# Optimization experiments

Hardware: AMD Instinct MI355X
Metric: run time of the kernel (lower is better)

The kernel has to match this reference:

```python
import jax, jax.numpy as jnp
import numpy as np

HIDDEN = 3584
H = 28          # num attention heads
KV = 4          # num key-value heads
HD = 128        # head dim
MROPE = [16, 24, 24]  # sum*2 == HD
EPS = 1e-6
S_TOT = 4096
N_SAMPLES = 4


def rmsnorm(x, w, eps=EPS):
    return x * jax.lax.rsqrt(jnp.mean(x * x, axis=-1, keepdims=True) + eps) * w


def rotate_half(x):
    x1, x2 = jnp.split(x, 2, axis=-1)
    return jnp.concatenate([-x2, x1], axis=-1)


def mrope_merge(t):
    # t: [3, S, HD] -> [S, HD], section i taken from rope axis i%3
    cuts = np.cumsum(np.array(MROPE) * 2)[:-1]
    parts = jnp.split(t, cuts, axis=-1)
    return jnp.concatenate([p[i % 3] for i, p in enumerate(parts)], axis=-1)


def setup_inputs() -> dict:
    key = jax.random.key(0)
    ks = iter(jax.random.split(key, 32))
    std = 0.02

    def w(shape):
        return jax.random.normal(next(ks), shape, dtype=jnp.float32) * std

    inp = {
        "packed_sequence": jax.random.normal(next(ks), (S_TOT, HIDDEN), dtype=jnp.float32),
        "packed_cos": jax.random.uniform(next(ks), (3, S_TOT, HD), dtype=jnp.float32, minval=-1.0, maxval=1.0),
        "packed_sin": jax.random.uniform(next(ks), (3, S_TOT, HD), dtype=jnp.float32, minval=-1.0, maxval=1.0),
    }
    # und / geo indices partition [0, S_TOT)
    inp["packed_und_token_indexes"] = jnp.arange(S_TOT // 2, dtype=jnp.int64 if jax.config.jax_enable_x64 else jnp.int32)
    inp["packed_geo_token_indexes"] = jnp.arange(S_TOT // 2, dtype=inp["packed_und_token_indexes"].dtype) + S_TOT // 2
    inp["sample_len"] = S_TOT // N_SAMPLES

    for tag in ("und", "geo"):
        inp[f"q_w_{tag}"] = w((H * HD, HIDDEN))
        inp[f"q_b_{tag}"] = jnp.zeros((H * HD,), jnp.float32)
        inp[f"k_w_{tag}"] = w((KV * HD, HIDDEN))
        inp[f"k_b_{tag}"] = jnp.zeros((KV * HD,), jnp.float32)
        inp[f"v_w_{tag}"] = w((KV * HD, HIDDEN))
        inp[f"v_b_{tag}"] = jnp.zeros((KV * HD,), jnp.float32)
        inp[f"o_w_{tag}"] = w((HIDDEN, H * HD))
        inp[f"q_norm_{tag}"] = jnp.ones((HD,), jnp.float32)
        inp[f"k_norm_{tag}"] = jnp.ones((HD,), jnp.float32)
    return inp


def reference(packed_sequence, packed_cos, packed_sin,
              q_w_und, q_b_und, k_w_und, k_b_und, v_w_und, v_b_und, o_w_und,
              q_norm_und, k_norm_und,
              q_w_geo, q_b_geo, k_w_geo, k_b_geo, v_w_geo, v_b_geo, o_w_geo,
              q_norm_geo, k_norm_geo,
              packed_und_token_indexes, packed_geo_token_indexes, sample_len):
    S, D = packed_sequence.shape
    G = H // KV
    und, geo = packed_und_token_indexes, packed_geo_token_indexes
    xu = packed_sequence[und]
    xg = packed_sequence[geo]

    def scatter(dim, fu, fg):
        out = jnp.zeros((S, dim), packed_sequence.dtype)
        return out.at[und].set(fu).at[geo].set(fg)

    # modality-routed QKV projections (gather -> gemm -> scatter)
    q = scatter(H * HD, xu @ q_w_und.T + q_b_und, xg @ q_w_geo.T + q_b_geo).reshape(S, H, HD)
    k = scatter(KV * HD, xu @ k_w_und.T + k_b_und, xg @ k_w_geo.T + k_b_geo).reshape(S, KV, HD)
    v = scatter(KV * HD, xu @ v_w_und.T + v_b_und, xg @ v_w_geo.T + v_b_geo).reshape(S, KV, HD)

    # per-modality QK RMSNorm
    qn = jnp.zeros_like(q).at[und].set(rmsnorm(q[und], q_norm_und)).at[geo].set(rmsnorm(q[geo], q_norm_geo))
    kn = jnp.zeros_like(k).at[und].set(rmsnorm(k[und], k_norm_und)).at[geo].set(rmsnorm(k[geo], k_norm_geo))

    # multimodal rotary embedding
    cos = mrope_merge(packed_cos)[:, None, :]  # [S,1,HD]
    sin = mrope_merge(packed_sin)[:, None, :]
    qr = qn * cos + rotate_half(qn) * sin
    kr = kn * cos + rotate_half(kn) * sin

    # block-diagonal causal attention over packed equal-length samples
    L = int(sample_len)
    B = S // L
    qb = qr.reshape(B, L, H, HD)
    kb = jnp.repeat(kr.reshape(B, L, KV, HD), G, axis=2)  # GQA expansion
    vb = jnp.repeat(v.reshape(B, L, KV, HD), G, axis=2)
    scores = jnp.einsum('blhd,bmhd->bhlm', qb, kb) / np.sqrt(HD).astype(np.float32)
    causal = jnp.tril(jnp.ones((L, L), bool))
    scores = jnp.where(causal, scores, jnp.finfo(scores.dtype).min)
    attn = jax.nn.softmax(scores, axis=-1)
    out = jnp.einsum('bhlm,bmhd->blhd', attn, vb).reshape(S, H * HD)

    # modality-routed output projection
    res = jnp.zeros((S, D), packed_sequence.dtype)
    res = res.at[und].set(out[und] @ o_w_und.T).at[geo].set(out[geo] @ o_w_geo.T)
    return res
```

## Files before the change

kernel.cpp:

```cpp
#include <hip/hip_runtime.h>
#include <hip/hip_bf16.h>
#include <stdint.h>

#define HIDDEN 3584
#define NH 28
#define NKV 4
#define HD 128
#define GQ (NH / NKV)
#define NQKV ((NH + 2 * NKV) * HD)
#define LSAMP 1024

typedef __bf16 bf16x8 __attribute__((ext_vector_type(8)));
typedef float f32x4 __attribute__((ext_vector_type(4)));

__device__ __forceinline__ unsigned short f2bf(float f) {
  unsigned int u = __float_as_uint(f);
  u += 0x7fffu + ((u >> 16) & 1u);
  return (unsigned short)(u >> 16);
}
__device__ __forceinline__ float bf2f(unsigned short h) {
  return __uint_as_float(((unsigned int)h) << 16);
}

__device__ __forceinline__ void gload16(const void* g, void* l) {
  __builtin_amdgcn_global_load_lds(
      (const __attribute__((address_space(1))) void*)g,
      (__attribute__((address_space(3))) void*)l, 16, 0, 0);
}

__global__ void build_maps_kernel(const int* __restrict__ und, const int* __restrict__ geo,
                                  int nu, int ng,
                                  int* __restrict__ row_of_token, int* __restrict__ tok_of_row,
                                  int* __restrict__ mod_of_token) {
  int i = blockIdx.x * 256 + threadIdx.x;
  if (i < nu) {
    int t = und[i];
    row_of_token[t] = i; tok_of_row[i] = t; mod_of_token[t] = 0;
  } else if (i < nu + ng) {
    int j = i - nu;
    int t = geo[j];
    row_of_token[t] = nu + j; tok_of_row[nu + j] = t; mod_of_token[t] = 1;
  }
}

struct Cvt8 {
  const float* src[8];
  unsigned short* dst[8];
  int cum[8];
};
__global__ void convert8_kernel(Cvt8 a, int tot4) {
  int i = blockIdx.x * blockDim.x + threadIdx.x;
  const int stride = gridDim.x * blockDim.x;
  for (; i < tot4; i += stride) {
    int seg = 0;
#pragma unroll
    for (int s2 = 1; s2 < 8; ++s2) seg += (i >= a.cum[s2]);
    const int off = i - a.cum[seg];
    float4 v = reinterpret_cast<const float4*>(a.src[seg])[off];
    reinterpret_cast<ushort4*>(a.dst[seg])[off] =
        make_ushort4(f2bf(v.x), f2bf(v.y), f2bf(v.z), f2bf(v.w));
  }
}

__global__ void gather_x_kernel(const float* __restrict__ X, const int* __restrict__ tok_of_row,
                                unsigned short* __restrict__ Xg) {
  const int r = blockIdx.x;
  const int tok = tok_of_row[r];
  const float4* src = reinterpret_cast<const float4*>(X + (size_t)tok * HIDDEN);
  ushort4* dst = reinterpret_cast<ushort4*>(Xg + (size_t)r * HIDDEN);
  for (int i = threadIdx.x; i < HIDDEN / 4; i += 256) {
    float4 v = src[i];
    dst[i] = make_ushort4(f2bf(v.x), f2bf(v.y), f2bf(v.z), f2bf(v.w));
  }
}

template <int OUTMODE, int NT, int WR, int WC, int NF>
__global__ __launch_bounds__(NT, (NT / 64 + 3) / 4)
void gemm2_kernel(const unsigned short* __restrict__ A,
                  const unsigned short* __restrict__ W0, const unsigned short* __restrict__ W1,
                  const float* __restrict__ qb0, const float* __restrict__ kb0, const float* __restrict__ vb0,
                  const float* __restrict__ qb1, const float* __restrict__ kb1, const float* __restrict__ vb1,
                  unsigned short* __restrict__ Obf, float* __restrict__ Of32,
                  const int* __restrict__ tok_of_row,
                  int nu, int ng, int N, int K, int NX, int NY) {
  constexpr int MF = 256 / WR / 16;
  constexpr int BN = WC * NF * 16;
  constexpr int BUFSZ = 32768 + BN * 128;
  constexpr int ACH = 2048;
  constexpr int BCH = BN * 8;
  __shared__ char lds[2 * BUFSZ];

  const int nwg = NX * NY * 2;
  int id = blockIdx.x + NX * (blockIdx.y + NY * blockIdx.z);
  {
    const int q = nwg >> 3, r = nwg & 7;
    const int xcd = id & 7, pos = id >> 3;
    id = (xcd < r ? xcd * (q + 1) : r * (q + 1) + (xcd - r) * q) + pos;
  }
  const int bx = id % NX;
  const int byz = id / NX;
  const int by = byz % NY;
  const int bz = byz / NY;

  const int baseRow = bz ? nu : 0;
  const int Mcount = bz ? ng : nu;
  const int mbase = by * 256;
  if (mbase >= Mcount) return;
  const unsigned short* W = bz ? W1 : W0;

  const int t = threadIdx.x;
  const int w = t >> 6, l = t & 63;
  const int l15 = l & 15, l4 = l >> 4;
  const int wr = w / WC, wc = w % WC;
  const int wrr = wr * (MF * 16), wcc = wc * (NF * 16);
  const int ncol0 = bx * BN;
  const int krev = w & 1;

  f32x4 acc[MF][NF] = {};

  const int nk = K >> 6;

  auto stage = [&](int bufIdx, int kt) {
    char* base = lds + bufIdx * BUFSZ;
    const int k0 = kt * 64;
#pragma unroll
    for (int c0 = 0; c0 < ACH; c0 += NT) {
      const int c = c0 + t;
      if (c < ACH) {
        const int row = c >> 3, slot = c & 7;
        const int srck = (slot ^ (row & 7)) << 3;
        int ar = mbase + row; if (ar >= Mcount) ar = Mcount - 1;
        gload16(A + (size_t)(baseRow + ar) * K + k0 + srck, base + c * 16);
      }
    }
#pragma unroll
    for (int c0 = 0; c0 < BCH; c0 += NT) {
      const int c = c0 + t;
      if (c < BCH) {
        const int row = c >> 3, slot = c & 7;
        const int srck = (slot ^ (row & 7)) << 3;
        gload16(W + (size_t)(ncol0 + row) * K + k0 + srck, base + 32768 + c * 16);
      }
    }
  };

  stage(0, 0);
  asm volatile("s_waitcnt vmcnt(0)\n\ts_barrier" ::: "memory");

  for (int kt = 0; kt < nk; ++kt) {
    char* Ab = lds + (kt & 1) * BUFSZ;
    char* Bb = Ab + 32768;

    if (kt + 1 < nk) stage((kt + 1) & 1, kt + 1);
    __builtin_amdgcn_sched_barrier(0);

#pragma unroll
    for (int ks = 0; ks < 2; ++ks) {
      const int kss = krev ? (1 - ks) : ks;
      bf16x8 af[MF], bfr[NF];
#pragma unroll
      for (int mf = 0; mf < MF; ++mf) {
        const int row = wrr + mf * 16 + l15;
        af[mf] = *reinterpret_cast<const bf16x8*>(Ab + row * 128 + (((kss * 4 + l4) ^ (row & 7)) << 4));
      }
#pragma unroll
      for (int nf = 0; nf < NF; ++nf) {
        const int row = wcc + nf * 16 + l15;
        bfr[nf] = *reinterpret_cast<const bf16x8*>(Bb + row * 128 + (((kss * 4 + l4) ^ (row & 7)) << 4));
      }
      __builtin_amdgcn_s_setprio(1);
#pragma unroll
      for (int mf = 0; mf < MF; ++mf)
#pragma unroll
        for (int nf = 0; nf < NF; ++nf)
          acc[mf][nf] = __builtin_amdgcn_mfma_f32_16x16x32_bf16(af[mf], bfr[nf], acc[mf][nf], 0, 0, 0);
      __builtin_amdgcn_s_setprio(0);
    }

    if (kt + 1 < nk) {
      asm volatile("s_waitcnt vmcnt(0)\n\ts_barrier" ::: "memory");
    }
  }

#pragma unroll
  for (int mf = 0; mf < MF; ++mf) {
#pragma unroll
    for (int rr = 0; rr < 4; ++rr) {
      const int ml = mbase + wrr + mf * 16 + l4 * 4 + rr;
      if (ml >= Mcount) continue;
      int trow = 0;
      if (OUTMODE == 1) trow = tok_of_row[baseRow + ml];
#pragma unroll
      for (int nf = 0; nf < NF; ++nf) {
        const int n = ncol0 + wcc + nf * 16 + l15;
        const float v = acc[mf][nf][rr];
        if (OUTMODE == 0) {
          const float* qb = bz ? qb1 : qb0;
          const float* kb = bz ? kb1 : kb0;
          const float* vb = bz ? vb1 : vb0;
          const float bias = (n < NH * HD) ? qb[n]
                              : ((n < (NH + NKV) * HD) ? kb[n - NH * HD] : vb[n - (NH + NKV) * HD]);
          Obf[(size_t)(baseRow + ml) * N + n] = f2bf(v + bias);
        } else {
          Of32[(size_t)trow * N + n] = v;
        }
      }
    }
  }
}

__global__ __launch_bounds__(64)
void norm_rope_kernel(const unsigned short* __restrict__ Y,
                      const int* __restrict__ row_of_token, const int* __restrict__ mod_of_token,
                      const float* __restrict__ pcos, const float* __restrict__ psin,
                      const float* __restrict__ qn_u, const float* __restrict__ kn_u,
                      const float* __restrict__ qn_g, const float* __restrict__ kn_g,
                      unsigned short* __restrict__ Qr,
                      unsigned short* __restrict__ Kr,
                      unsigned short* __restrict__ Vt,
                      int S) {
  const int s = blockIdx.x, l = threadIdx.x;
  const int g = l >> 4, l15 = l & 15;
  const int d0 = l15 * 8;
  const int axis = (d0 < 32) ? 0 : (d0 < 80 ? 1 : 2);
  const int r = row_of_token[s];
  const int m = mod_of_token[s];
  const float* qn = m ? qn_g : qn_u;
  const float* kn = m ? kn_g : kn_u;
  const bool hi = l15 >= 8;
  const float rsign = hi ? 1.f : -1.f;
  constexpr float SC = 0.08838834764831845f;

  float c8[8], s8[8], qw8[8], kw8[8];
  {
    const float* cp = pcos + ((size_t)axis * S + s) * HD + d0;
    const float* sp = psin + ((size_t)axis * S + s) * HD + d0;
#pragma unroll
    for (int j = 0; j < 8; ++j) { c8[j] = cp[j]; s8[j] = sp[j]; }
#pragma unroll
    for (int j = 0; j < 8; ++j) { qw8[j] = qn[d0 + j]; kw8[j] = kn[d0 + j]; }
  }
  const unsigned short* yrow = Y + (size_t)r * NQKV;

#pragma unroll
  for (int grp = 0; grp < 7; ++grp) {
    const int hh = grp * 4 + g;
    const bf16x8 y = *reinterpret_cast<const bf16x8*>(yrow + hh * HD + d0);
    float x[8], xw[8];
    float ss = 0.f;
#pragma unroll
    for (int j = 0; j < 8; ++j) { x[j] = bf2f(((unsigned short*)&y)[j]); ss += x[j] * x[j]; }
#pragma unroll
    for (int dd = 1; dd < 16; dd <<= 1) ss += __shfl_xor(ss, dd);
    const float rs = rsqrtf(ss * (1.f / 128.f) + 1e-6f) * SC;
#pragma unroll
    for (int j = 0; j < 8; ++j) xw[j] = x[j] * qw8[j];
    unsigned short o[8];
#pragma unroll
    for (int j = 0; j < 8; ++j) {
      const float xp = __shfl_xor(xw[j], 8);
      o[j] = f2bf(rs * (xw[j] * c8[j] + rsign * xp * s8[j]));
    }
    *reinterpret_cast<ushort4*>(Qr + ((size_t)hh * S + s) * HD + d0) = make_ushort4(o[0], o[1], o[2], o[3]);
    *reinterpret_cast<ushort4*>(Qr + ((size_t)hh * S + s) * HD + d0 + 4) = make_ushort4(o[4], o[5], o[6], o[7]);
  }

  {
    const int kh = g;
    const bf16x8 y = *reinterpret_cast<const bf16x8*>(yrow + (NH + kh) * HD + d0);
    float x[8], xw[8];
    float ss = 0.f;
#pragma unroll
    for (int j = 0; j < 8; ++j) { x[j] = bf2f(((unsigned short*)&y)[j]); ss += x[j] * x[j]; }
#pragma unroll
    for (int dd = 1; dd < 16; dd <<= 1) ss += __shfl_xor(ss, dd);
    const float rs = rsqrtf(ss * (1.f / 128.f) + 1e-6f);
#pragma unroll
    for (int j = 0; j < 8; ++j) xw[j] = x[j] * kw8[j];
    unsigned short o[8];
#pragma unroll
    for (int j = 0; j < 8; ++j) {
      const float xp = __shfl_xor(xw[j], 8);
      o[j] = f2bf(rs * (xw[j] * c8[j] + rsign * xp * s8[j]));
    }
    *reinterpret_cast<ushort4*>(Kr + ((size_t)kh * S + s) * HD + d0) = make_ushort4(o[0], o[1], o[2], o[3]);
    *reinterpret_cast<ushort4*>(Kr + ((size_t)kh * S + s) * HD + d0 + 4) = make_ushort4(o[4], o[5], o[6], o[7]);
  }

  {
    const int vh = g;
    const bf16x8 y = *reinterpret_cast<const bf16x8*>(yrow + (NH + NKV + vh) * HD + d0);
#pragma unroll
    for (int j = 0; j < 8; ++j)
      Vt[((size_t)(vh * HD + d0 + j)) * S + s] = ((unsigned short*)&y)[j];
  }
}

__global__ __launch_bounds__(448, 1)
void attn7_kernel(const unsigned short* __restrict__ Qr, const unsigned short* __restrict__ Kr,
                  const unsigned short* __restrict__ Vt, const int* __restrict__ row_of_token,
                  unsigned short* __restrict__ Og, int S) {
  __shared__ char lds[2 * 16384 + 2 * 16384 + 7 * 4608];
  const int kvh = blockIdx.y, b = blockIdx.z;
  const int t = threadIdx.x, w = t >> 6, l = t & 63;
  const int l15 = l & 15, l4 = l >> 4;
  const int h = kvh * GQ + w;
  const int sbase = b * LSAMP;
  char* Plds = lds + 65536 + w * 4608;

  auto stage = [&](int bufIdx, int kt) {
    char* Kb = lds + bufIdx * 16384;
    char* Vb = lds + 32768 + bufIdx * 16384;
    const int kb0 = sbase + kt * 64;
    for (int c = t; c < 1024; c += 448) {
      const int row = c >> 4, slot = c & 15;
      const int srcs = slot ^ (row & 15);
      gload16(Kr + ((size_t)kvh * S + kb0 + row) * HD + srcs * 8, Kb + c * 16);
    }
    for (int c = t; c < 1024; c += 448) {
      const int row = c >> 3, slot = c & 7;
      const int srcs = slot ^ (row & 7);
      gload16(Vt + (size_t)(kvh * HD + row) * S + kb0 + srcs * 8, Vb + c * 16);
    }
  };

  for (int pass = 0; pass < 2; ++pass) {
    const int q32 = pass ? (31 - blockIdx.x) : blockIdx.x;
    const int nkt = q32 / 2 + 1;

    bf16x8 aq[2][4];
#pragma unroll
    for (int fr = 0; fr < 2; ++fr) {
      const int qrow = sbase + q32 * 32 + fr * 16 + l15;
      const unsigned short* qp = Qr + ((size_t)h * S + qrow) * HD + l4 * 8;
#pragma unroll
      for (int kk = 0; kk < 4; ++kk) aq[fr][kk] = *reinterpret_cast<const bf16x8*>(qp + kk * 32);
    }
    f32x4 acc[2][8] = {};
    float mr[2][4], lr[2][4];
#pragma unroll
    for (int fr = 0; fr < 2; ++fr)
#pragma unroll
      for (int rr = 0; rr < 4; ++rr) { mr[fr][rr] = -INFINITY; lr[fr][rr] = 0.f; }

    stage(0, 0);
    asm volatile("s_waitcnt vmcnt(0)\n\ts_barrier" ::: "memory");

    for (int kt = 0; kt < nkt; ++kt) {
      char* Kb = lds + (kt & 1) * 16384;
      char* Vb = lds + 32768 + (kt & 1) * 16384;

      if (kt + 1 < nkt) stage((kt + 1) & 1, kt + 1);
      __builtin_amdgcn_sched_barrier(0);

      f32x4 sa[2][4] = {};
#pragma unroll
      for (int kk = 0; kk < 4; ++kk) {
        bf16x8 bk[4];
#pragma unroll
        for (int nf = 0; nf < 4; ++nf) {
          const int row = nf * 16 + l15;
          const int slot = kk * 4 + l4;
          bk[nf] = *reinterpret_cast<const bf16x8*>(Kb + row * 256 + ((slot ^ (row & 15)) << 4));
        }
#pragma unroll
        for (int fr = 0; fr < 2; ++fr)
#pragma unroll
          for (int nf = 0; nf < 4; ++nf)
            sa[fr][nf] = __builtin_amdgcn_mfma_f32_16x16x32_bf16(aq[fr][kk], bk[nf], sa[fr][nf], 0, 0, 0);
      }

#pragma unroll
      for (int fr = 0; fr < 2; ++fr) {
        const int qg = q32 * 32 + fr * 16 + l4 * 4;
#pragma unroll
        for (int nf = 0; nf < 4; ++nf) {
          const int cg = kt * 64 + nf * 16 + l15;
#pragma unroll
          for (int rr = 0; rr < 4; ++rr)
            if (cg > qg + rr) sa[fr][nf][rr] = -INFINITY;
        }
#pragma unroll
        for (int rr = 0; rr < 4; ++rr) {
          float mx = fmaxf(fmaxf(sa[fr][0][rr], sa[fr][1][rr]), fmaxf(sa[fr][2][rr], sa[fr][3][rr]));
          mx = fmaxf(mx, mr[fr][rr]);
#pragma unroll
          for (int dd = 1; dd < 16; dd <<= 1) mx = fmaxf(mx, __shfl_xor(mx, dd));
          const float alpha = __expf(mr[fr][rr] - mx);
          mr[fr][rr] = mx;
          float part = 0.f;
#pragma unroll
          for (int nf = 0; nf < 4; ++nf) {
            const float p = __expf(sa[fr][nf][rr] - mx);
            sa[fr][nf][rr] = p;
            part += p;
          }
          lr[fr][rr] = lr[fr][rr] * alpha + part;
#pragma unroll
          for (int nf2 = 0; nf2 < 8; ++nf2) acc[fr][nf2][rr] *= alpha;
        }
#pragma unroll
        for (int rr = 0; rr < 4; ++rr) {
          const int row = fr * 16 + l4 * 4 + rr;
#pragma unroll
          for (int nf = 0; nf < 4; ++nf)
            ((unsigned short*)(Plds + row * 144))[nf * 16 + l15] = f2bf(sa[fr][nf][rr]);
        }
      }

#pragma unroll
      for (int kk2 = 0; kk2 < 2; ++kk2) {
        bf16x8 ap[2];
#pragma unroll
        for (int fr = 0; fr < 2; ++fr)
          ap[fr] = *reinterpret_cast<const bf16x8*>(Plds + (fr * 16 + l15) * 144 + kk2 * 64 + l4 * 16);
#pragma unroll
        for (int nf2 = 0; nf2 < 8; ++nf2) {
          const int rowd = nf2 * 16 + l15;
          const int slot = kk2 * 4 + l4;
          const bf16x8 bv = *reinterpret_cast<const bf16x8*>(Vb + rowd * 128 + ((slot ^ (rowd & 7)) << 4));
#pragma unroll
          for (int fr = 0; fr < 2; ++fr)
            acc[fr][nf2] = __builtin_amdgcn_mfma_f32_16x16x32_bf16(ap[fr], bv, acc[fr][nf2], 0, 0, 0);
        }
      }

      if (kt + 1 < nkt) {
        asm volatile("s_waitcnt vmcnt(0)\n\ts_barrier" ::: "memory");
      }
    }

#pragma unroll
    for (int fr = 0; fr < 2; ++fr) {
#pragma unroll
      for (int rr = 0; rr < 4; ++rr) {
#pragma unroll
        for (int dd = 1; dd < 16; dd <<= 1) lr[fr][rr] += __shfl_xor(lr[fr][rr], dd);
        const float inv = 1.f / lr[fr][rr];
        const int srow = sbase + q32 * 32 + fr * 16 + l4 * 4 + rr;
        const int mrow = row_of_token[srow];
        unsigned short* orow = Og + (size_t)mrow * (NH * HD) + h * HD;
#pragma unroll
        for (int nf2 = 0; nf2 < 8; ++nf2) orow[nf2 * 16 + l15] = f2bf(acc[fr][nf2][rr] * inv);
      }
    }

    if (pass == 0) {
      asm volatile("s_waitcnt vmcnt(0) lgkmcnt(0)\n\ts_barrier" ::: "memory");
    }
  }
}

extern "C" void kernel_launch(void* const* d_in, const int* in_sizes, int n_in,
                              void* d_out, int out_size, void* d_ws, size_t ws_size,
                              hipStream_t stream) {
  const float* X = (const float*)d_in[0];
  const float* pcos = (const float*)d_in[1];
  const float* psin = (const float*)d_in[2];
  const int* und = (const int*)d_in[3];
  const int* geo = (const int*)d_in[4];
  const int nu = in_sizes[3], ng = in_sizes[4];
  const int S = in_sizes[0] / HIDDEN;

  const float* qw[2] = {(const float*)d_in[6], (const float*)d_in[15]};
  const float* qb[2] = {(const float*)d_in[7], (const float*)d_in[16]};
  const float* kw[2] = {(const float*)d_in[8], (const float*)d_in[17]};
  const float* kb[2] = {(const float*)d_in[9], (const float*)d_in[18]};
  const float* vw[2] = {(const float*)d_in[10], (const float*)d_in[19]};
  const float* vb[2] = {(const float*)d_in[11], (const float*)d_in[20]};
  const float* ow[2] = {(const float*)d_in[12], (const float*)d_in[21]};
  const float* qn[2] = {(const float*)d_in[13], (const float*)d_in[22]};
  const float* kn[2] = {(const float*)d_in[14], (const float*)d_in[23]};

  char* ws = (char*)d_ws;
  size_t off = 0;
  auto alloc = [&](size_t bytes) {
    char* p = ws + off;
    off = (off + bytes + 255) & ~(size_t)255;
    return p;
  };
  int* row_of_token = (int*)alloc((size_t)S * 4);
  int* tok_of_row = (int*)alloc((size_t)S * 4);
  int* mod_of_token = (int*)alloc((size_t)S * 4);
  unsigned short* Wqkv[2] = {(unsigned short*)alloc((size_t)NQKV * HIDDEN * 2),
                             (unsigned short*)alloc((size_t)NQKV * HIDDEN * 2)};
  unsigned short* Wo[2] = {(unsigned short*)alloc((size_t)HIDDEN * HIDDEN * 2),
                           (unsigned short*)alloc((size_t)HIDDEN * HIDDEN * 2)};
  unsigned short* Xg = (unsigned short*)alloc((size_t)S * HIDDEN * 2);
  unsigned short* Yqkv = (unsigned short*)alloc((size_t)S * NQKV * 2);
  unsigned short* Qr = (unsigned short*)alloc((size_t)NH * S * HD * 2);
  unsigned short* Kr = (unsigned short*)alloc((size_t)NKV * S * HD * 2);
  unsigned short* Vt = (unsigned short*)alloc((size_t)NKV * S * HD * 2);
  unsigned short* Og = (unsigned short*)alloc((size_t)S * NH * HD * 2);
  (void)ws_size; (void)n_in; (void)out_size;

  build_maps_kernel<<<(S + 255) / 256, 256, 0, stream>>>(und, geo, nu, ng,
                                                         row_of_token, tok_of_row, mod_of_token);
  {
    Cvt8 ca;
    const float* srcs[8] = {qw[0], kw[0], vw[0], ow[0], qw[1], kw[1], vw[1], ow[1]};
    unsigned short* dsts[8] = {
        Wqkv[0], Wqkv[0] + (size_t)NH * HD * HIDDEN, Wqkv[0] + (size_t)(NH + NKV) * HD * HIDDEN, Wo[0],
        Wqkv[1], Wqkv[1] + (size_t)NH * HD * HIDDEN, Wqkv[1] + (size_t)(NH + NKV) * HD * HIDDEN, Wo[1]};
    const int n4s[8] = {NH * HD * HIDDEN / 4, NKV * HD * HIDDEN / 4, NKV * HD * HIDDEN / 4, HIDDEN * HIDDEN / 4,
                        NH * HD * HIDDEN / 4, NKV * HD * HIDDEN / 4, NKV * HD * HIDDEN / 4, HIDDEN * HIDDEN / 4};
    int cum = 0;
    for (int i = 0; i < 8; ++i) { ca.src[i] = srcs[i]; ca.dst[i] = dsts[i]; ca.cum[i] = cum; cum += n4s[i]; }
    convert8_kernel<<<2048, 256, 0, stream>>>(ca, cum);
  }
  gather_x_kernel<<<S, 256, 0, stream>>>(X, tok_of_row, Xg);

  const int maxM = (nu > ng ? nu : ng);
  {
    const int NX = NQKV / 288, NY = (maxM + 255) / 256;
    gemm2_kernel<0, 768, 4, 3, 6><<<dim3(NX, NY, 2), 768, 0, stream>>>(
        Xg, Wqkv[0], Wqkv[1], qb[0], kb[0], vb[0], qb[1], kb[1], vb[1],
        Yqkv, nullptr, nullptr, nu, ng, NQKV, HIDDEN, NX, NY);
  }

  norm_rope_kernel<<<S, 64, 0, stream>>>(Yqkv, row_of_token, mod_of_token, pcos, psin,
                                         qn[0], kn[0], qn[1], kn[1], Qr, Kr, Vt, S);

  attn7_kernel<<<dim3(16, NKV, S / LSAMP), 448, 0, stream>>>(Qr, Kr, Vt, row_of_token, Og, S);

  {
    const int NX = HIDDEN / 224, NY = (maxM + 255) / 256;
    gemm2_kernel<1, 512, 4, 2, 7><<<dim3(NX, NY, 2), 512, 0, stream>>>(
        Og, Wo[0], Wo[1], nullptr, nullptr, nullptr, nullptr, nullptr, nullptr,
        nullptr, (float*)d_out, tok_of_row, nu, ng, HIDDEN, HIDDEN, NX, NY);
  }
}
```

Before: 392.6 us.

## Add 8-phase ping-pong GEMM schedule with XCD remap for QKV projection

Adds a new GEMM kernel for the QKV projection. Each K tile is split into four LDS-read/MFMA phases separated by barriers and setprio, and global prefetch of the tile two steps ahead is issued during the last phase. Workgroup IDs are remapped so consecutive tiles land on the same XCD. The aim is to overlap LDS reads and global loads with MFMA work and to improve L2 locality, at the cost of many more barriers and a hardcoded vmcnt literal.

```diff
diff --git a/kernel.cpp b/kernel.cpp
--- a/kernel.cpp
+++ b/kernel.cpp
@@ -71,6 +71,200 @@
   for (int i = threadIdx.x; i < HIDDEN / 4; i += 256) {
     float4 v = src[i];
     dst[i] = make_ushort4(f2bf(v.x), f2bf(v.y), f2bf(v.z), f2bf(v.w));
+  }
+}
+
+template <int OUTMODE, int NT, int WR, int WC, int NF, int NFA>
+__global__ __launch_bounds__(NT, (NT / 64 + 3) / 4)
+void gemm8p_kernel(const unsigned short* __restrict__ A,
+                   const unsigned short* __restrict__ W0, const unsigned short* __restrict__ W1,
+                   const float* __restrict__ qb0, const float* __restrict__ kb0, const float* __restrict__ vb0,
+                   const float* __restrict__ qb1, const float* __restrict__ kb1, const float* __restrict__ vb1,
+                   unsigned short* __restrict__ Obf, float* __restrict__ Of32,
+                   const int* __restrict__ tok_of_row,
+                   int nu, int ng, int N, int K, int NX, int NY) {
+  constexpr int MF = 256 / WR / 16;
+  constexpr int BN = WC * NF * 16;
+  constexpr int BUFSZ = 32768 + BN * 128;
+  constexpr int ACH = 2048;
+  constexpr int BCH = BN * 8;
+  constexpr int LA = (ACH + NT - 1) / NT;
+  constexpr int LB = (BCH + NT - 1) / NT;
+  static_assert(LA + LB == 6, "vmcnt literal assumes 6 loads/tile/thread");
+  __shared__ char lds[2 * BUFSZ];
+
+  const int nwg = NX * NY * 2;
+  int id = blockIdx.x + NX * (blockIdx.y + NY * blockIdx.z);
+  {
+    const int q = nwg >> 3, r = nwg & 7;
+    const int xcd = id & 7, pos = id >> 3;
+    id = (xcd < r ? xcd * (q + 1) : r * (q + 1) + (xcd - r) * q) + pos;
+  }
+  const int bx = id % NX;
+  const int byz = id / NX;
+  const int by = byz % NY;
+  const int bz = byz / NY;
+
+  const int baseRow = bz ? nu : 0;
+  const int Mcount = bz ? ng : nu;
+  const int mbase = by * 256;
+  if (mbase >= Mcount) return;
+  const unsigned short* W = bz ? W1 : W0;
+
+  const int t = threadIdx.x;
+  const int w = t >> 6, l = t & 63;
+  const int l15 = l & 15, l4 = l >> 4;
+  const int wr = w / WC, wc = w % WC;
+  const int wrr = wr * (MF * 16), wcc = wc * (NF * 16);
+  const int ncol0 = bx * BN;
+
+  f32x4 acc[MF][NF] = {};
+  const int nk = K >> 6;
+
+  auto stageA = [&](int bufIdx, int kt) {
+    char* base = lds + bufIdx * BUFSZ;
+    const int k0 = kt * 64;
+#pragma unroll
+    for (int i = 0; i < LA; ++i) {
+      int c = t + i * NT; if (c >= ACH) c -= ACH;
+      const int row = c >> 3, slot = c & 7;
+      const int srck = (slot ^ (row & 7)) << 3;
+      int ar = mbase + row; if (ar >= Mcount) ar = Mcount - 1;
+      gload16(A + (size_t)(baseRow + ar) * K + k0 + srck, base + c * 16);
+    }
+  };
+  auto stageB = [&](int bufIdx, int kt) {
+    char* base = lds + bufIdx * BUFSZ + 32768;
+    const int k0 = kt * 64;
+#pragma unroll
+    for (int i = 0; i < LB; ++i) {
+      int c = t + i * NT; if (c >= BCH) c -= BCH;
+      const int row = c >> 3, slot = c & 7;
+      const int srck = (slot ^ (row & 7)) << 3;
+      gload16(W + (size_t)(ncol0 + row) * K + k0 + srck, base + c * 16);
+    }
+  };
+
+  stageA(0, 0); stageB(0, 0);
+  if (nk > 1) {
+    stageA(1, 1); stageB(1, 1);
+    asm volatile("s_waitcnt vmcnt(6)\n\ts_barrier" ::: "memory");
+  } else {
+    asm volatile("s_waitcnt vmcnt(0)\n\ts_barrier" ::: "memory");
+  }
+
+  for (int kt = 0; kt < nk; ++kt) {
+    char* Ab = lds + (kt & 1) * BUFSZ;
+    char* Bb = Ab + 32768;
+    bf16x8 af[MF], b0[NFA], b1[NF - NFA];
+
+#pragma unroll
+    for (int mf = 0; mf < MF; ++mf) {
+      const int row = wrr + mf * 16 + l15;
+      af[mf] = *reinterpret_cast<const bf16x8*>(Ab + row * 128 + ((l4 ^ (row & 7)) << 4));
+    }
+#pragma unroll
+    for (int j = 0; j < NFA; ++j) {
+      const int row = wcc + j * 16 + l15;
+      b0[j] = *reinterpret_cast<const bf16x8*>(Bb + row * 128 + ((l4 ^ (row & 7)) << 4));
+    }
+    asm volatile("s_barrier" ::: "memory");
+    __builtin_amdgcn_sched_barrier(0);
+    __builtin_amdgcn_s_setprio(1);
+#pragma unroll
+    for (int mf = 0; mf < MF; ++mf)
+#pragma unroll
+      for (int j = 0; j < NFA; ++j)
+        acc[mf][j] = __builtin_amdgcn_mfma_f32_16x16x32_bf16(af[mf], b0[j], acc[mf][j], 0, 0, 0);
+    __builtin_amdgcn_s_setprio(0);
+    asm volatile("s_barrier" ::: "memory");
+
+#pragma unroll
+    for (int j = 0; j < NF - NFA; ++j) {
+      const int row = wcc + (NFA + j) * 16 + l15;
+      b1[j] = *reinterpret_cast<const bf16x8*>(Bb + row * 128 + ((l4 ^ (row & 7)) << 4));
+    }
+    asm volatile("s_barrier" ::: "memory");
+    __builtin_amdgcn_sched_barrier(0);
+    __builtin_amdgcn_s_setprio(1);
+#pragma unroll
+    for (int mf = 0; mf < MF; ++mf)
+#pragma unroll
+      for (int j = 0; j < NF - NFA; ++j)
+        acc[mf][NFA + j] = __builtin_amdgcn_mfma_f32_16x16x32_bf16(af[mf], b1[j], acc[mf][NFA + j], 0, 0, 0);
+    __builtin_amdgcn_s_setprio(0);
+    asm volatile("s_barrier" ::: "memory");
+
+#pragma unroll
+    for (int mf = 0; mf < MF; ++mf) {
+      const int row = wrr + mf * 16 + l15;
+      af[mf] = *reinterpret_cast<const bf16x8*>(Ab + row * 128 + (((4 + l4) ^ (row & 7)) << 4));
+    }
+#pragma unroll
+    for (int j = 0; j < NFA; ++j) {
+      const int row = wcc + j * 16 + l15;
+      b0[j] = *reinterpret_cast<const bf16x8*>(Bb + row * 128 + (((4 + l4) ^ (row & 7)) << 4));
+    }
+    asm volatile("s_barrier" ::: "memory");
+    __builtin_amdgcn_sched_barrier(0);
+    __builtin_amdgcn_s_setprio(1);
+#pragma unroll
+    for (int mf = 0; mf < MF; ++mf)
+#pragma unroll
+      for (int j = 0; j < NFA; ++j)
+        acc[mf][j] = __builtin_amdgcn_mfma_f32_16x16x32_bf16(af[mf], b0[j], acc[mf][j], 0, 0, 0);
+    __builtin_amdgcn_s_setprio(0);
+    asm volatile("s_barrier" ::: "memory");
+
+#pragma unroll
+    for (int j = 0; j < NF - NFA; ++j) {
+      const int row = wcc + (NFA + j) * 16 + l15;
+      b1[j] = *reinterpret_cast<const bf16x8*>(Bb + row * 128 + (((4 + l4) ^ (row & 7)) << 4));
+    }
+    asm volatile("s_barrier" ::: "memory");
+    __builtin_amdgcn_sched_barrier(0);
+    if (kt + 2 < nk) { stageA(kt & 1, kt + 2); stageB(kt & 1, kt + 2); }
+    __builtin_amdgcn_s_setprio(1);
+#pragma unroll
+    for (int mf = 0; mf < MF; ++mf)
+#pragma unroll
+      for (int j = 0; j < NF - NFA; ++j)
+        acc[mf][NFA + j] = __builtin_amdgcn_mfma_f32_16x16x32_bf16(af[mf], b1[j], acc[mf][NFA + j], 0, 0, 0);
+    __builtin_amdgcn_s_setprio(0);
+
+    if (kt + 1 < nk) {
+      if (kt + 2 < nk) {
+        asm volatile("s_waitcnt vmcnt(6)\n\ts_barrier" ::: "memory");
+      } else {
+        asm volatile("s_waitcnt vmcnt(0)\n\ts_barrier" ::: "memory");
+      }
+    }
+  }
+
+#pragma unroll
+  for (int mf = 0; mf < MF; ++mf) {
+#pragma unroll
+    for (int rr = 0; rr < 4; ++rr) {
+      const int ml = mbase + wrr + mf * 16 + l4 * 4 + rr;
+      if (ml >= Mcount) continue;
+      int trow = 0;
+      if (OUTMODE == 1) trow = tok_of_row[baseRow + ml];
+#pragma unroll
+      for (int nf = 0; nf < NF; ++nf) {
+        const int n = ncol0 + wcc + nf * 16 + l15;
+        const float v = acc[mf][nf][rr];
+        if (OUTMODE == 0) {
+          const float* qb = bz ? qb1 : qb0;
+          const float* kb = bz ? kb1 : kb0;
+          const float* vb = bz ? vb1 : vb0;
+          const float bias = (n < NH * HD) ? qb[n]
+                              : ((n < (NH + NKV) * HD) ? kb[n - NH * HD] : vb[n - (NH + NKV) * HD]);
+          Obf[(size_t)(baseRow + ml) * N + n] = f2bf(v + bias);
+        } else {
+          Of32[(size_t)trow * N + n] = v;
+        }
+      }
+    }
   }
 }
 
@@ -513,7 +707,7 @@
   const int maxM = (nu > ng ? nu : ng);
   {
     const int NX = NQKV / 288, NY = (maxM + 255) / 256;
-    gemm2_kernel<0, 768, 4, 3, 6><<<dim3(NX, NY, 2), 768, 0, stream>>>(
+    gemm8p_kernel<0, 768, 4, 3, 6, 3><<<dim3(NX, NY, 2), 768, 0, stream>>>(
         Xg, Wqkv[0], Wqkv[1], qb[0], kb[0], vb[0], qb[1], kb[1], vb[1],
         Yqkv, nullptr, nullptr, nu, ng, NQKV, HIDDEN, NX, NY);
   }
```

New measurement: 412.2 us. 5.0% more time.

## Fuse output-projection weight conversion into QKV GEMM main loop

Applied to the files above, without the earlier changes.

Removes the O-projection weight fp32-to-bf16 conversion from the standalone convert kernel and spreads it across the QKV GEMM's K-loop iterations, one float4 per thread per step. Idle workgroups beyond the M range do their share directly. The intent is to hide this memory-bound conversion under the compute-bound GEMM. The cost is added memory traffic and register pressure in the GEMM, plus extra waiting at the per-step vmcnt barrier.

```diff
diff --git a/kernel.cpp b/kernel.cpp
--- a/kernel.cpp
+++ b/kernel.cpp
@@ -74,7 +74,7 @@
   }
 }
 
-template <int OUTMODE, int NT, int WR, int WC, int NF>
+template <int OUTMODE, int NT, int WR, int WC, int NF, bool DOCVT>
 __global__ __launch_bounds__(NT, (NT / 64 + 3) / 4)
 void gemm2_kernel(const unsigned short* __restrict__ A,
                   const unsigned short* __restrict__ W0, const unsigned short* __restrict__ W1,
@@ -82,7 +82,10 @@
                   const float* __restrict__ qb1, const float* __restrict__ kb1, const float* __restrict__ vb1,
                   unsigned short* __restrict__ Obf, float* __restrict__ Of32,
                   const int* __restrict__ tok_of_row,
-                  int nu, int ng, int N, int K, int NX, int NY) {
+                  int nu, int ng, int N, int K, int NX, int NY,
+                  const float* __restrict__ cw0, const float* __restrict__ cw1,
+                  unsigned short* __restrict__ cd0, unsigned short* __restrict__ cd1,
+                  int wototal4) {
   constexpr int MF = 256 / WR / 16;
   constexpr int BN = WC * NF * 16;
   constexpr int BUFSZ = 32768 + BN * 128;
@@ -91,7 +94,8 @@
   __shared__ char lds[2 * BUFSZ];
 
   const int nwg = NX * NY * 2;
-  int id = blockIdx.x + NX * (blockIdx.y + NY * blockIdx.z);
+  const int flat0 = blockIdx.x + NX * (blockIdx.y + NY * blockIdx.z);
+  int id = flat0;
   {
     const int q = nwg >> 3, r = nwg & 7;
     const int xcd = id & 7, pos = id >> 3;
@@ -102,13 +106,36 @@
   const int by = byz % NY;
   const int bz = byz / NY;
 
+  const int t = threadIdx.x;
+  const int half4 = HIDDEN * HIDDEN / 4;
+  const size_t cvtStride = (size_t)nwg * NT;
+  const size_t mySlice = (size_t)flat0 * NT + t;
+
+  auto cvtLoad = [&](size_t ci, float4& v) {
+    if (ci < (size_t)half4) v = reinterpret_cast<const float4*>(cw0)[ci];
+    else v = reinterpret_cast<const float4*>(cw1)[ci - half4];
+  };
+  auto cvtStore = [&](size_t ci, const float4& v) {
+    ushort4 o = make_ushort4(f2bf(v.x), f2bf(v.y), f2bf(v.z), f2bf(v.w));
+    if (ci < (size_t)half4) reinterpret_cast<ushort4*>(cd0)[ci] = o;
+    else reinterpret_cast<ushort4*>(cd1)[ci - half4] = o;
+  };
+
   const int baseRow = bz ? nu : 0;
   const int Mcount = bz ? ng : nu;
   const int mbase = by * 256;
-  if (mbase >= Mcount) return;
+  if (mbase >= Mcount) {
+    if constexpr (DOCVT) {
+      const int nk = K >> 6;
+      for (int kt = 0; kt < nk; ++kt) {
+        const size_t ci = (size_t)kt * cvtStride + mySlice;
+        if (ci < (size_t)wototal4) { float4 v; cvtLoad(ci, v); cvtStore(ci, v); }
+      }
+    }
+    return;
+  }
   const unsigned short* W = bz ? W1 : W0;
 
-  const int t = threadIdx.x;
   const int w = t >> 6, l = t & 63;
   const int l15 = l & 15, l4 = l >> 4;
   const int wr = w / WC, wc = w % WC;
@@ -144,6 +171,9 @@
     }
   };
 
+  float4 cw;
+  size_t cprev = (size_t)-1;
+
   stage(0, 0);
   asm volatile("s_waitcnt vmcnt(0)\n\ts_barrier" ::: "memory");
 
@@ -152,6 +182,11 @@
     char* Bb = Ab + 32768;
 
     if (kt + 1 < nk) stage((kt + 1) & 1, kt + 1);
+    if constexpr (DOCVT) {
+      if (cprev != (size_t)-1) { cvtStore(cprev, cw); cprev = (size_t)-1; }
+      const size_t ci = (size_t)kt * cvtStride + mySlice;
+      if (ci < (size_t)wototal4) { cvtLoad(ci, cw); cprev = ci; }
+    }
     __builtin_amdgcn_sched_barrier(0);
 
 #pragma unroll
@@ -180,6 +215,10 @@
     if (kt + 1 < nk) {
       asm volatile("s_waitcnt vmcnt(0)\n\ts_barrier" ::: "memory");
     }
+  }
+
+  if constexpr (DOCVT) {
+    if (cprev != (size_t)-1) cvtStore(cprev, cw);
   }
 
 #pragma unroll
@@ -498,14 +537,16 @@
                                                          row_of_token, tok_of_row, mod_of_token);
   {
     Cvt8 ca;
-    const float* srcs[8] = {qw[0], kw[0], vw[0], ow[0], qw[1], kw[1], vw[1], ow[1]};
-    unsigned short* dsts[8] = {
-        Wqkv[0], Wqkv[0] + (size_t)NH * HD * HIDDEN, Wqkv[0] + (size_t)(NH + NKV) * HD * HIDDEN, Wo[0],
-        Wqkv[1], Wqkv[1] + (size_t)NH * HD * HIDDEN, Wqkv[1] + (size_t)(NH + NKV) * HD * HIDDEN, Wo[1]};
-    const int n4s[8] = {NH * HD * HIDDEN / 4, NKV * HD * HIDDEN / 4, NKV * HD * HIDDEN / 4, HIDDEN * HIDDEN / 4,
-                        NH * HD * HIDDEN / 4, NKV * HD * HIDDEN / 4, NKV * HD * HIDDEN / 4, HIDDEN * HIDDEN / 4};
+    const float* srcs[6] = {qw[0], kw[0], vw[0], qw[1], kw[1], vw[1]};
+    unsigned short* dsts[6] = {
+        Wqkv[0], Wqkv[0] + (size_t)NH * HD * HIDDEN, Wqkv[0] + (size_t)(NH + NKV) * HD * HIDDEN,
+        Wqkv[1], Wqkv[1] + (size_t)NH * HD * HIDDEN, Wqkv[1] + (size_t)(NH + NKV) * HD * HIDDEN};
+    const int n4s[6] = {NH * HD * HIDDEN / 4, NKV * HD * HIDDEN / 4, NKV * HD * HIDDEN / 4,
+                        NH * HD * HIDDEN / 4, NKV * HD * HIDDEN / 4, NKV * HD * HIDDEN / 4};
     int cum = 0;
-    for (int i = 0; i < 8; ++i) { ca.src[i] = srcs[i]; ca.dst[i] = dsts[i]; ca.cum[i] = cum; cum += n4s[i]; }
+    for (int i = 0; i < 6; ++i) { ca.src[i] = srcs[i]; ca.dst[i] = dsts[i]; ca.cum[i] = cum; cum += n4s[i]; }
+    ca.src[6] = srcs[5]; ca.dst[6] = dsts[5]; ca.cum[6] = cum;
+    ca.src[7] = srcs[5]; ca.dst[7] = dsts[5]; ca.cum[7] = cum;
     convert8_kernel<<<2048, 256, 0, stream>>>(ca, cum);
   }
   gather_x_kernel<<<S, 256, 0, stream>>>(X, tok_of_row, Xg);
@@ -513,9 +554,10 @@
   const int maxM = (nu > ng ? nu : ng);
   {
     const int NX = NQKV / 288, NY = (maxM + 255) / 256;
-    gemm2_kernel<0, 768, 4, 3, 6><<<dim3(NX, NY, 2), 768, 0, stream>>>(
+    gemm2_kernel<0, 768, 4, 3, 6, true><<<dim3(NX, NY, 2), 768, 0, stream>>>(
         Xg, Wqkv[0], Wqkv[1], qb[0], kb[0], vb[0], qb[1], kb[1], vb[1],
-        Yqkv, nullptr, nullptr, nu, ng, NQKV, HIDDEN, NX, NY);
+        Yqkv, nullptr, nullptr, nu, ng, NQKV, HIDDEN, NX, NY,
+        ow[0], ow[1], Wo[0], Wo[1], HIDDEN * HIDDEN / 2);
   }
 
   norm_rope_kernel<<<S, 64, 0, stream>>>(Yqkv, row_of_token, mod_of_token, pcos, psin,
@@ -525,8 +567,9 @@
 
   {
     const int NX = HIDDEN / 224, NY = (maxM + 255) / 256;
-    gemm2_kernel<1, 512, 4, 2, 7><<<dim3(NX, NY, 2), 512, 0, stream>>>(
+    gemm2_kernel<1, 512, 4, 2, 7, false><<<dim3(NX, NY, 2), 512, 0, stream>>>(
         Og, Wo[0], Wo[1], nullptr, nullptr, nullptr, nullptr, nullptr, nullptr,
-        nullptr, (float*)d_out, tok_of_row, nu, ng, HIDDEN, HIDDEN, NX, NY);
-  }
-}
+        nullptr, (float*)d_out, tok_of_row, nu, ng, HIDDEN, HIDDEN, NX, NY,
+        nullptr, nullptr, nullptr, nullptr, 0);
+  }
+}
```

Result: no change. 398.6 us (+1.5%).
